# Kernel optimization log

Measured on AMD Instinct MI355X. Metric: run time of the kernel, lower is better.

## Reference

```python
import jax, jax.numpy as jnp
import numpy as np

VOCAB = 32000
D_MODEL = 512
SEQ_TABLE = 2048
EPS = 1e-5


def layer_norm(x, gamma, beta):
    mu = jnp.mean(x, axis=-1, keepdims=True)
    var = jnp.mean(jnp.square(x - mu), axis=-1, keepdims=True)
    return (x - mu) * jax.lax.rsqrt(var + EPS) * gamma + beta


def setup_inputs() -> dict:
    key = jax.random.key(0)
    ks = jax.random.split(key, 12)
    s = 0.02
    d, h, V = D_MODEL, 4 * D_MODEL, VOCAB
    return {
        "x": jax.random.randint(ks[0], (4, 2048), 0, V, dtype=jnp.int64),
        "word_emb": jax.random.normal(ks[1], (V, d), jnp.float32) * s,
        "pos_emb": jax.random.normal(ks[2], (SEQ_TABLE, d), jnp.float32) * s,
        "Wq": jax.random.normal(ks[3], (d, d), jnp.float32) * s,
        "Wk": jax.random.normal(ks[4], (d, d), jnp.float32) * s,
        "Wv": jax.random.normal(ks[5], (d, d), jnp.float32) * s,
        "g1": jnp.ones((d,), jnp.float32),
        "b1": jnp.zeros((d,), jnp.float32),
        "w_ffn1": jax.random.normal(ks[6], (h, d), jnp.float32) * s,
        "b_ffn1": jnp.zeros((h,), jnp.float32),
        "w_ffn2": jax.random.normal(ks[7], (d, h), jnp.float32) * s,
        "b_ffn2": jnp.zeros((d,), jnp.float32),
        "g2": jnp.ones((d,), jnp.float32),
        "b2": jnp.zeros((d,), jnp.float32),
        "w_vocab": jax.random.normal(ks[8], (V, d), jnp.float32) * s,
        "b_vocab": jnp.zeros((V,), jnp.float32),
    }


def reference(x, word_emb, pos_emb, Wq, Wk, Wv, g1, b1,
              w_ffn1, b_ffn1, w_ffn2, b_ffn2, g2, b2, w_vocab, b_vocab):
    B, S = x.shape
    d_k = Wq.shape[0]
    # embeddings: word + learned positional
    emb = word_emb[x] + pos_emb[jnp.arange(S)][None, :, :]  # [B,S,d]
    # single-head causal attention (torch Linear: y = x @ W.T)
    Q = emb @ Wq.T
    K = emb @ Wk.T
    V = emb @ Wv.T
    scores = jnp.einsum('bqd,bkd->bqk', Q, K) / jnp.sqrt(jnp.float32(d_k))
    causal = jnp.tril(jnp.ones((S, S), bool))
    scores = jnp.where(causal[None], scores, -jnp.inf)
    attn = jax.nn.softmax(scores, axis=-1)
    context = jnp.einsum('bqk,bkd->bqd', attn, V)
    out1 = layer_norm(emb + context, g1, b1)
    ffn = jax.nn.relu(out1 @ w_ffn1.T + b_ffn1) @ w_ffn2.T + b_ffn2
    final = layer_norm(out1 + ffn, g2, b2)
    return final @ w_vocab.T + b_vocab  # [B,S,V]
```

## Files before the change

### kernel.cpp

```cpp
#include <hip/hip_runtime.h>
#include <hip/hip_bf16.h>

typedef __bf16 bf16;
typedef __attribute__((ext_vector_type(4))) __bf16 bf16x4;
typedef __attribute__((ext_vector_type(8))) __bf16 bf16x8;
typedef __attribute__((ext_vector_type(4))) float f32x4;

__device__ inline void gload_lds16(const bf16* g, bf16* l) {
    __builtin_amdgcn_global_load_lds(
        (const __attribute__((address_space(1))) void*)g,
        (__attribute__((address_space(3))) void*)l, 16, 0, 0);
}

struct CvtArgs {
    const float* src[6];
    bf16* dst[6];
    long n4[6];
    float scale[6];
};
__global__ void cvt_all(CvtArgs a) {
    int j = blockIdx.y;
    const float* __restrict__ src = a.src[j];
    bf16* __restrict__ dst = a.dst[j];
    long n4 = a.n4[j];
    float sc = a.scale[j];
    long i = (long)blockIdx.x * blockDim.x + threadIdx.x;
    long stride = (long)gridDim.x * blockDim.x;
    for (; i < n4; i += stride) {
        float4 v = ((const float4*)src)[i];
        bf16x4 o = { (bf16)(v.x * sc), (bf16)(v.y * sc), (bf16)(v.z * sc), (bf16)(v.w * sc) };
        ((bf16x4*)dst)[i] = o;
    }
}

__global__ void embed_kernel(const int* __restrict__ x, const float* __restrict__ we,
                             const float* __restrict__ pe, float* __restrict__ emb_f,
                             bf16* __restrict__ emb_b) {
    int row = blockIdx.x;
    int c   = threadIdx.x;
    int tok = x[row];
    int s   = row & 2047;
    float4 w = ((const float4*)we)[(long)tok * 128 + c];
    float4 p = ((const float4*)pe)[(long)s * 128 + c];
    float4 e = { w.x + p.x, w.y + p.y, w.z + p.z, w.w + p.w };
    ((float4*)emb_f)[(long)row * 128 + c] = e;
    bf16x4 eb = { (bf16)e.x, (bf16)e.y, (bf16)e.z, (bf16)e.w };
    ((bf16x4*)emb_b)[(long)row * 128 + c] = eb;
}

template<bool WF32, int C3, bool RBIAS>
__global__ void ln_kernel(const float* __restrict__ a, const float* __restrict__ b,
                          const float* __restrict__ c, const float* __restrict__ rb,
                          const float* __restrict__ g, const float* __restrict__ bb,
                          float* __restrict__ of, bf16* __restrict__ ob) {
    int row = blockIdx.x;
    int t   = threadIdx.x;
    float4 xa = ((const float4*)a)[(long)row * 128 + t];
    float4 xb = ((const float4*)b)[(long)row * 128 + t];
    float4 xv = { xa.x + xb.x, xa.y + xb.y, xa.z + xb.z, xa.w + xb.w };
    if (C3 == 2 || (C3 == 1 && (row & 2047) >= 1024)) {
        float4 xc = ((const float4*)c)[(long)row * 128 + t];
        xv.x += xc.x; xv.y += xc.y; xv.z += xc.z; xv.w += xc.w;
    }
    if (RBIAS) {
        float4 rv = ((const float4*)rb)[t];
        xv.x += rv.x; xv.y += rv.y; xv.z += rv.z; xv.w += rv.w;
    }
    float s  = xv.x + xv.y + xv.z + xv.w;
    float sq = xv.x * xv.x + xv.y * xv.y + xv.z * xv.z + xv.w * xv.w;
    #pragma unroll
    for (int o = 32; o > 0; o >>= 1) {
        s  += __shfl_xor(s, o);
        sq += __shfl_xor(sq, o);
    }
    __shared__ float rs[2], rq[2];
    int wid = t >> 6;
    if ((t & 63) == 0) { rs[wid] = s; rq[wid] = sq; }
    __syncthreads();
    s = rs[0] + rs[1]; sq = rq[0] + rq[1];
    float mu   = s * (1.0f / 512.0f);
    float var  = sq * (1.0f / 512.0f) - mu * mu;
    float rstd = rsqrtf(var + 1e-5f);
    float4 gv = ((const float4*)g)[t];
    float4 bv = ((const float4*)bb)[t];
    float4 y = { (xv.x - mu) * rstd * gv.x + bv.x,
                 (xv.y - mu) * rstd * gv.y + bv.y,
                 (xv.z - mu) * rstd * gv.z + bv.z,
                 (xv.w - mu) * rstd * gv.w + bv.w };
    if (WF32) ((float4*)of)[(long)row * 128 + t] = y;
    bf16x4 yb = { (bf16)y.x, (bf16)y.y, (bf16)y.z, (bf16)y.w };
    ((bf16x4*)ob)[(long)row * 128 + t] = yb;
}

__global__ void softmax_causal(const float* __restrict__ sc, bf16* __restrict__ pr) {
    int row = blockIdx.x;
    int z = row >> 11, q = row & 2047;
    const float* srow = sc + ((long)z * 2048 + q) * 2048;
    bf16*        prow = pr + ((long)z * 2048 + q) * 2048;
    int t = threadIdx.x;
    float v[8];
    int c0 = t * 8;
    if (t <= (q >> 3)) {
        float4 v0 = ((const float4*)srow)[t * 2];
        float4 v1 = ((const float4*)srow)[t * 2 + 1];
        v[0] = v0.x; v[1] = v0.y; v[2] = v0.z; v[3] = v0.w;
        v[4] = v1.x; v[5] = v1.y; v[6] = v1.z; v[7] = v1.w;
    } else {
        #pragma unroll
        for (int j = 0; j < 8; j++) v[j] = -1e30f;
    }
    float mx = -1e30f;
    #pragma unroll
    for (int j = 0; j < 8; j++) {
        if (c0 + j > q) v[j] = -1e30f;
        mx = fmaxf(mx, v[j]);
    }
    int lane = t & 63, wid = t >> 6;
    #pragma unroll
    for (int o = 32; o > 0; o >>= 1) mx = fmaxf(mx, __shfl_xor(mx, o));
    __shared__ float redm[4], reds[4];
    if (lane == 0) redm[wid] = mx;
    __syncthreads();
    mx = fmaxf(fmaxf(redm[0], redm[1]), fmaxf(redm[2], redm[3]));
    float p[8]; float sum = 0.f;
    #pragma unroll
    for (int j = 0; j < 8; j++) {
        p[j] = (c0 + j <= q) ? __expf(v[j] - mx) : 0.f;
        sum += p[j];
    }
    #pragma unroll
    for (int o = 32; o > 0; o >>= 1) sum += __shfl_xor(sum, o);
    if (lane == 0) reds[wid] = sum;
    __syncthreads();
    sum = reds[0] + reds[1] + reds[2] + reds[3];
    float inv = 1.0f / sum;
    int wlim = ((q >> 7) + 1) * 128;
    if (c0 < wlim) {
        bf16x8 o;
        #pragma unroll
        for (int j = 0; j < 8; j++) o[j] = (bf16)(p[j] * inv);
        *(bf16x8*)&prow[c0] = o;
    }
}

enum { EPI_F32 = 0, EPI_BF16 = 1, EPI_VT = 2, EPI_BIAS_RELU_BF16 = 3, EPI_BIAS_F32 = 4,
       EPI_QKV = 5, EPI_BIAS_F32_NT = 6 };
enum { ZB_BATCH = 0, ZB_PV = 1 };

template<int EPI, bool CAUSAL_SKIP, bool CAUSAL_K, bool XCD, int ZMODE>
__global__ __launch_bounds__(256)
void gemm_bt(const bf16* __restrict__ A, const bf16* __restrict__ B,
             float* __restrict__ Cf, bf16* __restrict__ Cb,
             const float* __restrict__ bias, float scale,
             int M, int N, int K, int Krow, long sA, long sB, long sC) {
    int br, bc;
    if (XCD) {
        int nwg = gridDim.x * gridDim.y;
        int lin = blockIdx.y * gridDim.x + blockIdx.x;
        lin = (lin & 7) * (nwg >> 3) + (lin >> 3);
        br = lin / gridDim.x; bc = lin - br * gridDim.x;
    } else { br = blockIdx.y; bc = blockIdx.x; }
    int z = blockIdx.z;
    int Kext = K;
    if (ZMODE == ZB_BATCH) {
        A += (long)z * sA; B += (long)z * sB; Cf += (long)z * sC;
    } else if (ZMODE == ZB_PV) {
        int batch = z >> 1, chunk = z & 1;
        A += (long)batch * sA; B += (long)batch * sB;
        Cf += (long)chunk * (8192L * 512) + (long)batch * sC;
        int keff = min(K, (br + 1) * 128);
        int lo = chunk * 1024;
        if (keff <= lo) return;
        A += lo; B += lo;
        Kext = min(keff, lo + 1024) - lo;
    }
    if (CAUSAL_SKIP && bc > br) return;
    if (CAUSAL_K) Kext = min(Kext, (br + 1) * 128);
    __shared__ bf16 As[128 * 64];
    __shared__ bf16 Bs[128 * 64];
    int tid = threadIdx.x;
    int lane = tid & 63, wid = tid >> 6;
    int wm = (wid >> 1) * 64, wn = (wid & 1) * 64;
    f32x4 acc[4][4] = {};
    int rowA0 = br * 128, colB0 = bc * 128;
    int rsub = lane >> 3;
    int csub = ((lane & 7) ^ rsub) * 8;
    int rdsw = (lane & 7) * 8;
    for (int kt = 0; kt < Kext; kt += 64) {
        const bf16* Ag = A + (long)rowA0 * Krow + kt;
        const bf16* Bg = B + (long)colB0 * Krow + kt;
        #pragma unroll
        for (int i = 0; i < 4; i++) {
            int seg = wid * 4 + i;
            int r = seg * 8 + rsub;
            gload_lds16(&Ag[(long)r * Krow + csub], &As[seg * 512]);
            gload_lds16(&Bg[(long)r * Krow + csub], &Bs[seg * 512]);
        }
        __syncthreads();
        #pragma unroll
        for (int kk = 0; kk < 2; kk++) {
            bf16x8 af[4], bfr[4];
            int ko = (kk * 32 + (lane >> 4) * 8) ^ rdsw;
            #pragma unroll
            for (int m = 0; m < 4; m++) af[m]  = *(const bf16x8*)&As[(wm + m * 16 + (lane & 15)) * 64 + ko];
            #pragma unroll
            for (int n = 0; n < 4; n++) bfr[n] = *(const bf16x8*)&Bs[(wn + n * 16 + (lane & 15)) * 64 + ko];
            #pragma unroll
            for (int m = 0; m < 4; m++)
                #pragma unroll
                for (int n = 0; n < 4; n++)
                    acc[m][n] = __builtin_amdgcn_mfma_f32_16x16x32_bf16(af[m], bfr[n], acc[m][n], 0, 0, 0);
        }
        __syncthreads();
    }
    #pragma unroll
    for (int m = 0; m < 4; m++) {
        #pragma unroll
        for (int n = 0; n < 4; n++) {
            #pragma unroll
            for (int j = 0; j < 4; j++) {
                int row = rowA0 + wm + m * 16 + (lane >> 4) * 4 + j;
                int col = colB0 + wn + n * 16 + (lane & 15);
                float v = acc[m][n][j];
                if (EPI == EPI_F32) {
                    Cf[(long)row * N + col] = v;
                } else if (EPI == EPI_BF16) {
                    Cb[(long)row * N + col] = (bf16)(v * scale);
                } else if (EPI == EPI_VT) {
                    int b = row >> 11, k = row & 2047;
                    Cb[((long)b * 512 + col) * 2048 + k] = (bf16)v;
                } else if (EPI == EPI_BIAS_RELU_BF16) {
                    float y = fmaxf(v + bias[col], 0.0f);
                    Cb[(long)row * N + col] = (bf16)y;
                } else if (EPI == EPI_BIAS_F32) {
                    Cf[(long)row * N + col] = v + bias[col];
                }
            }
        }
    }
}

template<int EPI, bool XCD, bool CSKIP, int BANDW, int NT>
__global__ __launch_bounds__(512)
void gemm256(const bf16* __restrict__ A, const bf16* __restrict__ B,
             float* __restrict__ Cf, bf16* __restrict__ Cb,
             const float* __restrict__ bias, int N, int K,
             long sA, long sB, long sC) {
    int br, bc;
    if (XCD) {
        int nwg = gridDim.x * gridDim.y;
        int lin = blockIdx.y * gridDim.x + blockIdx.x;
        lin = (lin & 7) * (nwg >> 3) + (lin >> 3);
        if (BANDW > 0) {
            int per = BANDW * gridDim.y;
            int band = lin / per, w2 = lin - band * per;
            br = w2 / BANDW; bc = band * BANDW + (w2 - br * BANDW);
        } else {
            br = lin / gridDim.x; bc = lin - br * gridDim.x;
        }
    } else { br = blockIdx.y; bc = blockIdx.x; }
    if (CSKIP && bc > br) return;
    int z = blockIdx.z;
    A  += (long)z * sA;
    B  += (long)z * sB;
    Cf += (long)z * sC;
    __shared__ bf16 lds[2][2][256 * 64];
    int tid = threadIdx.x;
    int lane = tid & 63, wid = tid >> 6;
    int wm2 = wid >> 2, wn4 = wid & 3;
    long rowA0 = (long)br * 256, colB0 = (long)bc * 256;
    int rsub = lane >> 3;
    int csw  = ((lane & 7) ^ rsub) * 8;
    int l15 = lane & 15;
    int rdxor = (lane & 7) << 3;
    int kbase = (lane >> 4) * 8;
    const bf16* Abase = A + rowA0 * K;
    const bf16* Bbase = B + colB0 * K;
    f32x4 acc[8][4] = {};

    auto stage = [&](int t) {
        int buf = t & 1;
        const bf16* Ag = Abase + t * 64;
        const bf16* Bg = Bbase + t * 64;
        #pragma unroll
        for (int i = 0; i < 4; i++) {
            int seg = wid * 4 + i;
            long r = seg * 8 + rsub;
            gload_lds16(&Ag[r * K + csw], &lds[buf][0][seg * 512]);
        }
        #pragma unroll
        for (int i = 0; i < 4; i++) {
            int seg = wid * 4 + i;
            long r = seg * 8 + rsub;
            gload_lds16(&Bg[r * K + csw], &lds[buf][1][seg * 512]);
        }
    };

    stage(0);
    stage(1);

    for (int t = 0; t < NT; t++) {
        int buf = t & 1;
        if (t == NT - 1) asm volatile("s_waitcnt vmcnt(0)" ::: "memory");
        else             asm volatile("s_waitcnt vmcnt(8)" ::: "memory");
        __builtin_amdgcn_s_barrier();
        const bf16* As = lds[buf][0];
        const bf16* Bs = lds[buf][1];
        bf16x8 bfr[2][4], af[2][4];
        #pragma unroll
        for (int kk = 0; kk < 2; kk++)
            #pragma unroll
            for (int n = 0; n < 4; n++) {
                int r = wn4 * 64 + n * 16 + l15;
                bfr[kk][n] = *(const bf16x8*)&Bs[r * 64 + ((kk * 32 + kbase) ^ rdxor)];
            }
        #pragma unroll
        for (int kk = 0; kk < 2; kk++)
            #pragma unroll
            for (int m = 0; m < 4; m++) {
                int r = wm2 * 128 + m * 16 + l15;
                af[kk][m] = *(const bf16x8*)&As[r * 64 + ((kk * 32 + kbase) ^ rdxor)];
            }
        __builtin_amdgcn_s_setprio(1);
        #pragma unroll
        for (int kk = 0; kk < 2; kk++)
            #pragma unroll
            for (int m = 0; m < 4; m++)
                #pragma unroll
                for (int n = 0; n < 4; n++)
                    acc[m][n] = __builtin_amdgcn_mfma_f32_16x16x32_bf16(af[kk][m], bfr[kk][n], acc[m][n], 0, 0, 0);
        __builtin_amdgcn_s_setprio(0);
        #pragma unroll
        for (int kk = 0; kk < 2; kk++)
            #pragma unroll
            for (int m = 0; m < 4; m++) {
                int r = wm2 * 128 + 64 + m * 16 + l15;
                af[kk][m] = *(const bf16x8*)&As[r * 64 + ((kk * 32 + kbase) ^ rdxor)];
            }
        asm volatile("s_waitcnt lgkmcnt(0)" ::: "memory");
        __builtin_amdgcn_sched_barrier(0);
        __builtin_amdgcn_s_barrier();
        if (t + 2 < NT) stage(t + 2);
        __builtin_amdgcn_s_setprio(1);
        #pragma unroll
        for (int kk = 0; kk < 2; kk++)
            #pragma unroll
            for (int m = 0; m < 4; m++)
                #pragma unroll
                for (int n = 0; n < 4; n++)
                    acc[4 + m][n] = __builtin_amdgcn_mfma_f32_16x16x32_bf16(af[kk][m], bfr[kk][n], acc[4 + m][n], 0, 0, 0);
        __builtin_amdgcn_s_setprio(0);
    }

    if constexpr (EPI == EPI_QKV) {
        int region = (int)(colB0 >> 9);
        if (region < 2) {
            bf16* dst = Cb + (long)region * (8192L * 512);
            int cb = ((int)colB0 & 511) + wn4 * 64;
            #pragma unroll
            for (int m = 0; m < 8; m++)
                #pragma unroll
                for (int n = 0; n < 4; n++)
                    #pragma unroll
                    for (int j = 0; j < 4; j++) {
                        long row = rowA0 + wm2 * 128 + m * 16 + (lane >> 4) * 4 + j;
                        int c = cb + n * 16 + l15;
                        dst[row * 512 + c] = (bf16)acc[m][n][j];
                    }
        } else {
            bf16* vtb = Cb + 2L * 8192 * 512;
            int cb = ((int)colB0 - 1024) + wn4 * 64;
            #pragma unroll
            for (int m = 0; m < 8; m++)
                #pragma unroll
                for (int n = 0; n < 4; n++) {
                    long k0 = rowA0 + wm2 * 128 + m * 16 + (lane >> 4) * 4;
                    long b = k0 >> 11, k = k0 & 2047;
                    int c = cb + n * 16 + l15;
                    bf16x4 pk = { (bf16)acc[m][n][0], (bf16)acc[m][n][1],
                                  (bf16)acc[m][n][2], (bf16)acc[m][n][3] };
                    *(bf16x4*)&vtb[(b * 512 + c) * 2048 + k] = pk;
                }
        }
    } else {
        #pragma unroll
        for (int m = 0; m < 8; m++) {
            #pragma unroll
            for (int n = 0; n < 4; n++) {
                #pragma unroll
                for (int j = 0; j < 4; j++) {
                    long row = rowA0 + wm2 * 128 + m * 16 + (lane >> 4) * 4 + j;
                    long col = colB0 + wn4 * 64 + n * 16 + l15;
                    float v = acc[m][n][j];
                    if (EPI == EPI_BIAS_F32) {
                        Cf[row * N + col] = v + bias[col];
                    } else if (EPI == EPI_BIAS_F32_NT) {
                        __builtin_nontemporal_store(v + bias[col], &Cf[row * N + col]);
                    } else if (EPI == EPI_BIAS_RELU_BF16) {
                        Cb[row * N + col] = (bf16)fmaxf(v + bias[col], 0.0f);
                    } else if (EPI == EPI_F32) {
                        Cf[row * N + col] = v;
                    }
                }
            }
        }
    }
}

template<int BANDB>
__global__ __launch_bounds__(256)
void gemm128v(const bf16* __restrict__ A, const bf16* __restrict__ B,
              float* __restrict__ C, const float* __restrict__ bias,
              int N, int K) {
    const int NBR = 64;
    const int NT  = 8;
    int nwg = gridDim.x;
    int lin = blockIdx.x;
    lin = (lin & 7) * (nwg >> 3) + (lin >> 3);
    int per = BANDB * NBR;
    int band = lin / per, w2 = lin - band * per;
    int br = w2 / BANDB, bc = band * BANDB + (w2 - br * BANDB);

    __shared__ bf16 lds[2][2][128 * 64];
    int tid = threadIdx.x;
    int lane = tid & 63, wid = tid >> 6;
    int wm = (wid >> 1) * 64, wn = (wid & 1) * 64;
    int rsub = lane >> 3;
    int csub = ((lane & 7) ^ rsub) * 8;
    int rdsw = (lane & 7) * 8;
    long rowA0 = (long)br * 128, colB0 = (long)bc * 128;
    const bf16* Abase = A + rowA0 * K;
    const bf16* Bbase = B + colB0 * K;
    f32x4 acc[4][4] = {};

    auto stage = [&](int t) {
        int buf = t & 1;
        const bf16* Ag = Abase + t * 64;
        const bf16* Bg = Bbase + t * 64;
        #pragma unroll
        for (int i = 0; i < 4; i++) {
            int seg = wid * 4 + i;
            long r = seg * 8 + rsub;
            gload_lds16(&Ag[r * K + csub], &lds[buf][0][seg * 512]);
        }
        #pragma unroll
        for (int i = 0; i < 4; i++) {
            int seg = wid * 4 + i;
            long r = seg * 8 + rsub;
            gload_lds16(&Bg[r * K + csub], &lds[buf][1][seg * 512]);
        }
    };

    stage(0);
    stage(1);

    for (int t = 0; t < NT; t++) {
        int buf = t & 1;
        if (t == NT - 1) asm volatile("s_waitcnt vmcnt(0)" ::: "memory");
        else             asm volatile("s_waitcnt vmcnt(8)" ::: "memory");
        __builtin_amdgcn_s_barrier();
        const bf16* As = lds[buf][0];
        const bf16* Bs = lds[buf][1];
        __builtin_amdgcn_s_setprio(1);
        #pragma unroll
        for (int kk = 0; kk < 2; kk++) {
            bf16x8 af[4], bfr[4];
            int ko = (kk * 32 + (lane >> 4) * 8) ^ rdsw;
            #pragma unroll
            for (int m = 0; m < 4; m++) af[m]  = *(const bf16x8*)&As[(wm + m * 16 + (lane & 15)) * 64 + ko];
            #pragma unroll
            for (int n = 0; n < 4; n++) bfr[n] = *(const bf16x8*)&Bs[(wn + n * 16 + (lane & 15)) * 64 + ko];
            #pragma unroll
            for (int m = 0; m < 4; m++)
                #pragma unroll
                for (int n = 0; n < 4; n++)
                    acc[m][n] = __builtin_amdgcn_mfma_f32_16x16x32_bf16(af[m], bfr[n], acc[m][n], 0, 0, 0);
        }
        __builtin_amdgcn_s_setprio(0);
        asm volatile("s_waitcnt lgkmcnt(0)" ::: "memory");
        __builtin_amdgcn_sched_barrier(0);
        __builtin_amdgcn_s_barrier();
        if (t + 2 < NT) stage(t + 2);
    }

    #pragma unroll
    for (int m = 0; m < 4; m++) {
        #pragma unroll
        for (int n = 0; n < 4; n++) {
            int col = (int)colB0 + wn + n * 16 + (lane & 15);
            float bcol = bias[col];
            #pragma unroll
            for (int j = 0; j < 4; j++) {
                long row = rowA0 + wm + m * 16 + (lane >> 4) * 4 + j;
                __builtin_nontemporal_store(acc[m][n][j] + bcol, &C[row * N + col]);
            }
        }
    }
}

extern "C" void kernel_launch(void* const* d_in, const int* in_sizes, int n_in,
                              void* d_out, int out_size, void* d_ws, size_t ws_size,
                              hipStream_t stream) {
    const int*   x       = (const int*)d_in[0];
    const float* word_emb = (const float*)d_in[1];
    const float* pos_emb  = (const float*)d_in[2];
    const float* Wq = (const float*)d_in[3];
    const float* Wk = (const float*)d_in[4];
    const float* Wv = (const float*)d_in[5];
    const float* g1 = (const float*)d_in[6];
    const float* b1 = (const float*)d_in[7];
    const float* w_ffn1 = (const float*)d_in[8];
    const float* b_ffn1 = (const float*)d_in[9];
    const float* w_ffn2 = (const float*)d_in[10];
    const float* b_ffn2 = (const float*)d_in[11];
    const float* g2 = (const float*)d_in[12];
    const float* b2 = (const float*)d_in[13];
    const float* w_vocab = (const float*)d_in[14];
    const float* b_vocab = (const float*)d_in[15];
    float* out = (float*)d_out;

    char* w = (char*)d_ws;
    auto alloc = [&](size_t bytes) { char* p = w; w += (bytes + 255) & ~255ULL; return p; };
    bf16* wqb   = (bf16*)alloc(512 * 512 * 2);
    bf16* wkb   = (bf16*)alloc(512 * 512 * 2);
    bf16* wvb   = (bf16*)alloc(512 * 512 * 2);
    bf16* w1b   = (bf16*)alloc(2048 * 512 * 2);
    bf16* w2b   = (bf16*)alloc(512 * 2048 * 2);
    bf16* wvocb = (bf16*)alloc((size_t)32000 * 512 * 2);
    float* embf = (float*)alloc((size_t)8192 * 512 * 4);
    bf16* embb  = (bf16*)alloc((size_t)8192 * 512 * 2);
    bf16* qb    = (bf16*)alloc((size_t)8192 * 512 * 2);
    bf16* kb    = (bf16*)alloc((size_t)8192 * 512 * 2);
    bf16* vt    = (bf16*)alloc((size_t)8192 * 512 * 2);
    float* scores = (float*)alloc((size_t)4 * 2048 * 2048 * 4);
    bf16* probs = (bf16*)alloc((size_t)4 * 2048 * 2048 * 2);
    float* ctx  = (float*)alloc((size_t)8192 * 512 * 4);
    float* pv1  = (float*)alloc((size_t)8192 * 512 * 4);
    float* out1f = (float*)alloc((size_t)8192 * 512 * 4);
    float* ffn2f = (float*)alloc((size_t)8192 * 512 * 4);
    float* ffn2b = (float*)alloc((size_t)8192 * 512 * 4);
    bf16* ffn1b = (bf16*)scores;
    bf16* out1b = kb;
    bf16* finalb = embb;

    const float qscale = 0.044194173824159216f;

    CvtArgs ca;
    ca.src[0] = Wq;      ca.dst[0] = wqb;   ca.n4[0] = 512 * 512 / 4;          ca.scale[0] = qscale;
    ca.src[1] = Wk;      ca.dst[1] = wkb;   ca.n4[1] = 512 * 512 / 4;          ca.scale[1] = 1.0f;
    ca.src[2] = Wv;      ca.dst[2] = wvb;   ca.n4[2] = 512 * 512 / 4;          ca.scale[2] = 1.0f;
    ca.src[3] = w_ffn1;  ca.dst[3] = w1b;   ca.n4[3] = 2048 * 512 / 4;         ca.scale[3] = 1.0f;
    ca.src[4] = w_ffn2;  ca.dst[4] = w2b;   ca.n4[4] = 512 * 2048 / 4;         ca.scale[4] = 1.0f;
    ca.src[5] = w_vocab; ca.dst[5] = wvocb; ca.n4[5] = (long)32000 * 512 / 4;  ca.scale[5] = 1.0f;
    cvt_all<<<dim3(256, 6), 256, 0, stream>>>(ca);

    embed_kernel<<<8192, 128, 0, stream>>>(x, word_emb, pos_emb, embf, embb);

    gemm256<EPI_QKV, true, false, 0, 8><<<dim3(6, 32, 1), 512, 0, stream>>>(
        embb, wqb, nullptr, qb, nullptr, 1536, 512, 0, 0, 0);

    gemm256<EPI_F32, true, true, 0, 8><<<dim3(8, 8, 4), 512, 0, stream>>>(
        qb, kb, scores, nullptr, nullptr, 2048, 512,
        (long)2048 * 512, (long)2048 * 512, (long)2048 * 2048);

    softmax_causal<<<8192, 256, 0, stream>>>(scores, probs);

    gemm_bt<EPI_F32, false, false, false, ZB_PV><<<dim3(4, 16, 8), 256, 0, stream>>>(
        probs, vt, ctx, nullptr, nullptr, 1.0f, 2048, 512, 2048, 2048,
        (long)2048 * 2048, (long)512 * 2048, (long)2048 * 512);

    ln_kernel<true, 1, false><<<8192, 128, 0, stream>>>(
        embf, ctx, pv1, nullptr, g1, b1, out1f, out1b);

    gemm256<EPI_BIAS_RELU_BF16, true, false, 0, 8><<<dim3(8, 32, 1), 512, 0, stream>>>(
        out1b, w1b, nullptr, ffn1b, b_ffn1, 2048, 512, 0, 0, 0);

    gemm_bt<EPI_F32, false, false, false, ZB_BATCH><<<dim3(4, 64, 2), 256, 0, stream>>>(
        ffn1b, w2b, ffn2f, nullptr, nullptr, 1.0f, 8192, 512, 1024, 2048,
        1024, 1024, 8192L * 512);

    ln_kernel<false, 2, true><<<8192, 128, 0, stream>>>(
        out1f, ffn2f, ffn2b, b_ffn2, g2, b2, nullptr, finalb);

    gemm128v<10><<<16000, 256, 0, stream>>>(finalb, wvocb, out, b_vocab, 32000, 512);
}
```

Measured before the change: 535.5 us.

## Fuse embed with weight conversion, split PV into four K chunks, retile QK^T

Merges the weight-to-bf16 conversion and the embedding gather into one launch by giving each job its own block range. Splits the causal PV split-K into four 512-wide chunks instead of two, writing partials to two extra buffers. LayerNorm 1 sums only the partials that exist for each row's position. The QK^T scores GEMM moves from the 256-tile kernel to the 128-tile gemm_bt with causal tile skipping. The aims are fewer launches, better load balance over the causal triangle and more parallel blocks, at the cost of extra partial-buffer traffic and smaller tiles.

After: 529.7 us. Within noise of the previous version (-1.1%).

```diff
diff --git a/kernel.cpp b/kernel.cpp
--- a/kernel.cpp
+++ b/kernel.cpp
@@ -18,34 +18,38 @@
     long n4[6];
     float scale[6];
 };
-__global__ void cvt_all(CvtArgs a) {
-    int j = blockIdx.y;
-    const float* __restrict__ src = a.src[j];
-    bf16* __restrict__ dst = a.dst[j];
-    long n4 = a.n4[j];
-    float sc = a.scale[j];
-    long i = (long)blockIdx.x * blockDim.x + threadIdx.x;
-    long stride = (long)gridDim.x * blockDim.x;
-    for (; i < n4; i += stride) {
-        float4 v = ((const float4*)src)[i];
-        bf16x4 o = { (bf16)(v.x * sc), (bf16)(v.y * sc), (bf16)(v.z * sc), (bf16)(v.w * sc) };
-        ((bf16x4*)dst)[i] = o;
-    }
-}
-
-__global__ void embed_kernel(const int* __restrict__ x, const float* __restrict__ we,
-                             const float* __restrict__ pe, float* __restrict__ emb_f,
-                             bf16* __restrict__ emb_b) {
-    int row = blockIdx.x;
-    int c   = threadIdx.x;
-    int tok = x[row];
-    int s   = row & 2047;
-    float4 w = ((const float4*)we)[(long)tok * 128 + c];
-    float4 p = ((const float4*)pe)[(long)s * 128 + c];
-    float4 e = { w.x + p.x, w.y + p.y, w.z + p.z, w.w + p.w };
-    ((float4*)emb_f)[(long)row * 128 + c] = e;
-    bf16x4 eb = { (bf16)e.x, (bf16)e.y, (bf16)e.z, (bf16)e.w };
-    ((bf16x4*)emb_b)[(long)row * 128 + c] = eb;
+__global__ void embed_cvt(CvtArgs a, const int* __restrict__ x,
+                          const float* __restrict__ we, const float* __restrict__ pe,
+                          float* __restrict__ emb_f, bf16* __restrict__ emb_b) {
+    int b = blockIdx.x;
+    int tid = threadIdx.x;
+    if (b < 4096) {
+        int row = b * 2 + (tid >> 7);
+        int c = tid & 127;
+        int tok = x[row];
+        int s = row & 2047;
+        float4 w = ((const float4*)we)[(long)tok * 128 + c];
+        float4 p = ((const float4*)pe)[(long)s * 128 + c];
+        float4 e = { w.x + p.x, w.y + p.y, w.z + p.z, w.w + p.w };
+        ((float4*)emb_f)[(long)row * 128 + c] = e;
+        bf16x4 eb = { (bf16)e.x, (bf16)e.y, (bf16)e.z, (bf16)e.w };
+        ((bf16x4*)emb_b)[(long)row * 128 + c] = eb;
+    } else {
+        int bb = b - 4096;
+        int j  = bb >> 8;
+        int bx = bb & 255;
+        const float* __restrict__ src = a.src[j];
+        bf16* __restrict__ dst = a.dst[j];
+        long n4 = a.n4[j];
+        float sc = a.scale[j];
+        long i = (long)bx * 256 + tid;
+        long stride = 256 * 256;
+        for (; i < n4; i += stride) {
+            float4 v = ((const float4*)src)[i];
+            bf16x4 o = { (bf16)(v.x * sc), (bf16)(v.y * sc), (bf16)(v.z * sc), (bf16)(v.w * sc) };
+            ((bf16x4*)dst)[i] = o;
+        }
+    }
 }
 
 template<bool WF32, int C3, bool RBIAS>
@@ -58,7 +62,16 @@
     float4 xa = ((const float4*)a)[(long)row * 128 + t];
     float4 xb = ((const float4*)b)[(long)row * 128 + t];
     float4 xv = { xa.x + xb.x, xa.y + xb.y, xa.z + xb.z, xa.w + xb.w };
-    if (C3 == 2 || (C3 == 1 && (row & 2047) >= 1024)) {
+    if (C3 == 1) {
+        int r = row & 2047;
+        #pragma unroll
+        for (int k = 1; k <= 3; k++) {
+            if (r >= k * 512) {
+                float4 xc = ((const float4*)(c + (long)(k - 1) * 8192 * 512))[(long)row * 128 + t];
+                xv.x += xc.x; xv.y += xc.y; xv.z += xc.z; xv.w += xc.w;
+            }
+        }
+    } else if (C3 == 2) {
         float4 xc = ((const float4*)c)[(long)row * 128 + t];
         xv.x += xc.x; xv.y += xc.y; xv.z += xc.z; xv.w += xc.w;
     }
@@ -165,14 +178,14 @@
     if (ZMODE == ZB_BATCH) {
         A += (long)z * sA; B += (long)z * sB; Cf += (long)z * sC;
     } else if (ZMODE == ZB_PV) {
-        int batch = z >> 1, chunk = z & 1;
+        int batch = z >> 2, chunk = z & 3;
         A += (long)batch * sA; B += (long)batch * sB;
         Cf += (long)chunk * (8192L * 512) + (long)batch * sC;
         int keff = min(K, (br + 1) * 128);
-        int lo = chunk * 1024;
+        int lo = chunk * 512;
         if (keff <= lo) return;
         A += lo; B += lo;
-        Kext = min(keff, lo + 1024) - lo;
+        Kext = min(keff, lo + 512) - lo;
     }
     if (CAUSAL_SKIP && bc > br) return;
     if (CAUSAL_K) Kext = min(Kext, (br + 1) * 128);
@@ -536,12 +549,15 @@
     bf16* probs = (bf16*)alloc((size_t)4 * 2048 * 2048 * 2);
     float* ctx  = (float*)alloc((size_t)8192 * 512 * 4);
     float* pv1  = (float*)alloc((size_t)8192 * 512 * 4);
+    float* pv2  = (float*)alloc((size_t)8192 * 512 * 4);
+    float* pv3  = (float*)alloc((size_t)8192 * 512 * 4);
     float* out1f = (float*)alloc((size_t)8192 * 512 * 4);
     float* ffn2f = (float*)alloc((size_t)8192 * 512 * 4);
     float* ffn2b = (float*)alloc((size_t)8192 * 512 * 4);
     bf16* ffn1b = (bf16*)scores;
     bf16* out1b = kb;
     bf16* finalb = embb;
+    (void)pv2; (void)pv3;
 
     const float qscale = 0.044194173824159216f;
 
@@ -552,20 +568,18 @@
     ca.src[3] = w_ffn1;  ca.dst[3] = w1b;   ca.n4[3] = 2048 * 512 / 4;         ca.scale[3] = 1.0f;
     ca.src[4] = w_ffn2;  ca.dst[4] = w2b;   ca.n4[4] = 512 * 2048 / 4;         ca.scale[4] = 1.0f;
     ca.src[5] = w_vocab; ca.dst[5] = wvocb; ca.n4[5] = (long)32000 * 512 / 4;  ca.scale[5] = 1.0f;
-    cvt_all<<<dim3(256, 6), 256, 0, stream>>>(ca);
-
-    embed_kernel<<<8192, 128, 0, stream>>>(x, word_emb, pos_emb, embf, embb);
+    embed_cvt<<<5632, 256, 0, stream>>>(ca, x, word_emb, pos_emb, embf, embb);
 
     gemm256<EPI_QKV, true, false, 0, 8><<<dim3(6, 32, 1), 512, 0, stream>>>(
         embb, wqb, nullptr, qb, nullptr, 1536, 512, 0, 0, 0);
 
-    gemm256<EPI_F32, true, true, 0, 8><<<dim3(8, 8, 4), 512, 0, stream>>>(
-        qb, kb, scores, nullptr, nullptr, 2048, 512,
+    gemm_bt<EPI_F32, true, false, false, ZB_BATCH><<<dim3(16, 16, 4), 256, 0, stream>>>(
+        qb, kb, scores, nullptr, nullptr, 1.0f, 2048, 2048, 512, 512,
         (long)2048 * 512, (long)2048 * 512, (long)2048 * 2048);
 
     softmax_causal<<<8192, 256, 0, stream>>>(scores, probs);
 
-    gemm_bt<EPI_F32, false, false, false, ZB_PV><<<dim3(4, 16, 8), 256, 0, stream>>>(
+    gemm_bt<EPI_F32, false, false, false, ZB_PV><<<dim3(4, 16, 16), 256, 0, stream>>>(
         probs, vt, ctx, nullptr, nullptr, 1.0f, 2048, 512, 2048, 2048,
         (long)2048 * 2048, (long)512 * 2048, (long)2048 * 512);
 
```
